# Optimization experiments

Measured on AMD Instinct MI355X. Metric: run time of the kernel, lower is better.

## Reference

```python
import jax, jax.numpy as jnp
import numpy as np

HIDDEN = 512
HEADS = 8
DK = HIDDEN // HEADS  # 64
NEG = -1000000000.0


def setup_inputs() -> dict:
    key = jax.random.key(0)
    ks = jax.random.split(key, 16)
    B, S = 4, 1024
    inp = {
        "q": jax.random.normal(ks[0], (B, S, HIDDEN), jnp.float32),
        "k": jax.random.normal(ks[1], (B, S, HIDDEN), jnp.float32),
        "v": jax.random.normal(ks[2], (B, S, HIDDEN), jnp.float32),
        "attn_bias": jax.random.normal(ks[3], (B, HEADS, S, S), jnp.float32),
        "graph_mask": jax.random.randint(ks[4], (B, 1, S, S), 0, 2, jnp.int32),
        "subsq_mask": jax.random.normal(ks[5], (B, 1, S, S), jnp.float32),
        # linear params (PyTorch Linear: y = x @ W.T + b)
        "Wq": jax.random.normal(ks[6], (HIDDEN, HIDDEN), jnp.float32) * 0.02,
        "bq": jnp.zeros((HIDDEN,), jnp.float32),
        "Wk": jax.random.normal(ks[7], (HIDDEN, HIDDEN), jnp.float32) * 0.02,
        "bk": jnp.zeros((HIDDEN,), jnp.float32),
        "Wv": jax.random.normal(ks[8], (HIDDEN, HIDDEN), jnp.float32) * 0.02,
        "bv": jnp.zeros((HIDDEN,), jnp.float32),
        "Wo": jax.random.normal(ks[9], (HIDDEN, HIDDEN), jnp.float32) * 0.02,
        "bo": jnp.zeros((HIDDEN,), jnp.float32),
    }
    return inp


def reference(q, k, v, attn_bias, graph_mask, subsq_mask, Wq, bq, Wk, bk, Wv, bv, Wo, bo):
    B, S, _ = q.shape
    scale = DK ** (-0.5)
    # projections -> [B, heads, S, d]
    qh = (q @ Wq.T + bq).reshape(B, S, HEADS, DK).transpose(0, 2, 1, 3)
    kh = (k @ Wk.T + bk).reshape(B, S, HEADS, DK).transpose(0, 2, 1, 3)
    vh = (v @ Wv.T + bv).reshape(B, S, HEADS, DK).transpose(0, 2, 1, 3)
    # scaled scores [B, heads, S, S]
    scores = jnp.einsum('bhqd,bhkd->bhqk', qh * scale, kh)
    zero = graph_mask == 0  # [B,1,S,S], broadcasts over heads
    bias = jnp.where(zero, NEG, attn_bias)
    x = scores + bias + subsq_mask
    x = jnp.where(zero, NEG, x)
    attn = jax.nn.softmax(x, axis=-1)
    out = jnp.einsum('bhqk,bhkd->bhqd', attn, vh)
    out = out.transpose(0, 2, 1, 3).reshape(B, S, HEADS * DK)
    return out @ Wo.T + bo
```

## Files before the change

### kernel.cpp

```cpp
#include <hip/hip_runtime.h>

#define HIDDEN 512
#define HEADS 8
#define DK 64
#define S_ 1024
#define NEGV -1000000000.0f

typedef _Float16 half8 __attribute__((ext_vector_type(8)));
typedef _Float16 half4 __attribute__((ext_vector_type(4)));
typedef _Float16 half2_t __attribute__((ext_vector_type(2)));
typedef float f32x4 __attribute__((ext_vector_type(4)));
typedef float f32x2 __attribute__((ext_vector_type(2)));
typedef int i32x4 __attribute__((ext_vector_type(4)));

__device__ __forceinline__ void gload16(const void* g, void* l) {
  __builtin_amdgcn_global_load_lds(
      (const __attribute__((address_space(1))) unsigned int*)g,
      (__attribute__((address_space(3))) unsigned int*)l, 16, 0, 0);
}

__global__ __launch_bounds__(256) void cvt3(const float* __restrict__ a0,
                                            const float* __restrict__ a1,
                                            const float* __restrict__ a2,
                                            _Float16* o0, _Float16* o1, _Float16* o2) {
  const float* src = blockIdx.y == 0 ? a0 : (blockIdx.y == 1 ? a1 : a2);
  _Float16* dst = blockIdx.y == 0 ? o0 : (blockIdx.y == 1 ? o1 : o2);
  int i = (blockIdx.x * 256 + threadIdx.x) * 4;
  float4 v = *(const float4*)(src + i);
  half4 h = {(_Float16)v.x, (_Float16)v.y, (_Float16)v.z, (_Float16)v.w};
  *(half4*)(dst + i) = h;
}

__global__ __launch_bounds__(256) void cvt4(const float* __restrict__ a0,
                                            const float* __restrict__ a1,
                                            const float* __restrict__ a2,
                                            const float* __restrict__ a3,
                                            _Float16* o0, _Float16* o1, _Float16* o2, _Float16* o3) {
  const float* src = blockIdx.y == 0 ? a0 : (blockIdx.y == 1 ? a1 : (blockIdx.y == 2 ? a2 : a3));
  _Float16* dst = blockIdx.y == 0 ? o0 : (blockIdx.y == 1 ? o1 : (blockIdx.y == 2 ? o2 : o3));
  int i = (blockIdx.x * 256 + threadIdx.x) * 4;
  float4 v = *(const float4*)(src + i);
  half4 h = {(_Float16)v.x, (_Float16)v.y, (_Float16)v.z, (_Float16)v.w};
  *(half4*)(dst + i) = h;
}

__global__ __launch_bounds__(256) void fusemask(const int* __restrict__ gm,
                                                const float* __restrict__ sq,
                                                _Float16* __restrict__ msk) {
  int i = (blockIdx.x * 256 + threadIdx.x) * 4;
  i32x4 g = *(const i32x4*)(gm + i);
  f32x4 s = *(const f32x4*)(sq + i);
  half4 o;
#pragma unroll
  for (int j = 0; j < 4; j++)
    o[j] = (_Float16)(g[j] == 0 ? -30000.0f : s[j]);
  *(half4*)(msk + i) = o;
}

__global__ __launch_bounds__(256) void proj_qkv2(
    const _Float16* __restrict__ q16, const _Float16* __restrict__ k16,
    const _Float16* __restrict__ v16,
    const _Float16* __restrict__ wq, const _Float16* __restrict__ wk,
    const _Float16* __restrict__ wv,
    const float* __restrict__ bq, const float* __restrict__ bk,
    const float* __restrict__ bv,
    _Float16* __restrict__ qh, _Float16* __restrict__ kh, _Float16* __restrict__ vt) {
  int m0 = blockIdx.x * 64;
  int nb = blockIdx.y;
  int which = nb >> 3;
  int n0 = (nb & 7) * 64;
  const _Float16* X = which == 0 ? q16 : (which == 1 ? k16 : v16);
  const _Float16* W = which == 0 ? wq : (which == 1 ? wk : wv);
  const float* bias = which == 0 ? bq : (which == 1 ? bk : bv);

  int tid = threadIdx.x;
  int wave = tid >> 6, lane = tid & 63;
  int r16 = lane & 15, quad = lane >> 4;

  __shared__ __align__(16) char SM[25600];
  _Float16(*T)[72] = (_Float16(*)[72])(SM + 16384);

  int rl = lane >> 2;
  int ku = lane & 3;
  int kup = ku ^ ((rl >> 1) & 3);

  const _Float16* Xg = X + (size_t)(m0 + wave * 16 + rl) * HIDDEN + kup * 8;
  const _Float16* Wg = W + (size_t)(n0 + wave * 16 + rl) * HIDDEN + kup * 8;

  auto stage = [&](int k0, int buf) __attribute__((always_inline)) {
    gload16(Xg + k0, SM + buf * 4096 + wave * 1024);
    gload16(Wg + k0, SM + 8192 + buf * 4096 + wave * 1024);
  };

  f32x4 acc[4] = {};
  stage(0, 0);
  int sw = (r16 >> 1) & 3;

  for (int t = 0; t < 16; t++) {
    int k0n = (t < 15) ? (t + 1) * 32 : 0;
    stage(k0n, (t + 1) & 1);
    asm volatile("s_waitcnt vmcnt(2)" ::: "memory");
    __builtin_amdgcn_sched_barrier(0);
    __builtin_amdgcn_s_barrier();

    int buf = t & 1;
    const _Float16* XT = (const _Float16*)(SM + buf * 4096);
    const _Float16* WT = (const _Float16*)(SM + 8192 + buf * 4096);
    half8 a = *(const half8*)&XT[(wave * 16 + r16) * 32 + ((quad ^ sw) << 3)];
#pragma unroll
    for (int nt = 0; nt < 4; nt++) {
      half8 bfr = *(const half8*)&WT[(nt * 16 + r16) * 32 + ((quad ^ sw) << 3)];
      acc[nt] = __builtin_amdgcn_mfma_f32_16x16x32_f16(a, bfr, acc[nt], 0, 0, 0);
    }
    __builtin_amdgcn_s_barrier();
  }
  asm volatile("s_waitcnt vmcnt(0)" ::: "memory");

  if (which < 2) {
    _Float16* OUT = which == 0 ? qh : kh;
    float scale = which == 0 ? 0.125f : 1.0f;
#pragma unroll
    for (int nt = 0; nt < 4; nt++) {
      int gcol = n0 + nt * 16 + r16;
      float bv_ = bias[gcol];
      int h = gcol >> 6, d = gcol & 63;
#pragma unroll
      for (int r = 0; r < 4; r++) {
        int grow = m0 + wave * 16 + quad * 4 + r;
        int bb = grow >> 10, s = grow & 1023;
        float val = (acc[nt][r] + bv_) * scale;
        OUT[((bb * HEADS + h) * S_ + s) * DK + d] = (_Float16)val;
      }
    }
  } else {
#pragma unroll
    for (int nt = 0; nt < 4; nt++) {
      int lc = nt * 16 + r16;
      float bv_ = bias[n0 + lc];
#pragma unroll
      for (int r = 0; r < 4; r++) {
        int lr = wave * 16 + quad * 4 + r;
        T[lr][lc] = (_Float16)(acc[nt][r] + bv_);
      }
    }
    __syncthreads();
    int dl = tid >> 2;
    int s4 = (tid & 3) * 16;
    _Float16 tmp[16];
#pragma unroll
    for (int i = 0; i < 16; i++) tmp[i] = T[s4 + i][dl];
    int h = n0 >> 6;
    int bb = m0 >> 10;
    int s0 = m0 & 1023;
    _Float16* p = vt + ((bb * HEADS + h) * DK + dl) * S_ + s0 + s4;
    *(half8*)(p) = *(half8*)(tmp);
    *(half8*)(p + 8) = *(half8*)(tmp + 8);
  }
}

__global__ __launch_bounds__(256) void attn8(
    const _Float16* __restrict__ qh, const _Float16* __restrict__ kh,
    const _Float16* __restrict__ vt,
    const float* __restrict__ attn_bias, const _Float16* __restrict__ msk,
    _Float16* __restrict__ ao) {
  int id = blockIdx.x;
  int bh = (((id >> 3) & 3) << 3) | (id & 7);
  int qtile = id >> 5;
  int b = bh >> 3, h = bh & 7;
  int tid = threadIdx.x;
  int wave = tid >> 6, lane = tid & 63;
  int col = lane & 15, quad = lane >> 4;
  int q0w = qtile * 64 + wave * 16;
  int q = q0w + col;
  int xr = col & 7;
  int lr8 = lane >> 3;
  int u8 = (lane & 7) ^ lr8;

  __shared__ __align__(16) char SMEM[46080];
  _Float16* Klds = (_Float16*)SMEM;
  _Float16* Vlds = (_Float16*)(SMEM + 8192);
  char* bws = SMEM + 16384 + wave * 4096;
  char* mws = SMEM + 32768 + wave * 2048;
  float* Bw = (float*)bws;
  _Float16* Mw = (_Float16*)mws;
  unsigned(*P2)[16][20] = (unsigned(*)[16][20])(SMEM + 40960);

  const _Float16* Q = qh + ((size_t)bh * S_ + q) * DK;
  const _Float16* K = kh + (size_t)bh * S_ * DK;
  const _Float16* V = vt + (size_t)bh * DK * S_;
  const float* BIrow = attn_bias + ((size_t)bh * S_ + q0w) * S_;
  const _Float16* MSrow = msk + ((size_t)b * S_ + q0w) * S_;

  half8 qf0 = *(const half8*)(Q + quad * 8);
  half8 qf1 = *(const half8*)(Q + 32 + quad * 8);

  f32x4 acc[4] = {};
  float m_r = -1e38f, l_r = 0.0f;

  for (int t = 0; t < 16; t++) {
    int kb = t * 64;
#pragma unroll
    for (int cc = 0; cc < 2; cc++) {
      int c = wave + cc * 4;
      int row = c * 8 + lr8;
      gload16(K + (size_t)(kb + row) * DK + u8 * 8, SMEM + c * 1024);
    }
#pragma unroll
    for (int cc = 0; cc < 2; cc++) {
      int c = wave + cc * 4;
      int row = c * 8 + lr8;
      gload16(V + (size_t)row * S_ + kb + u8 * 8, SMEM + 8192 + c * 1024);
    }
#pragma unroll
    for (int c = 0; c < 4; c++) {
      int row = c * 4 + (lane >> 4);
      int ju = (lane & 15) ^ (row & 7);
      gload16(BIrow + (size_t)row * S_ + kb + ju * 4, bws + c * 1024);
    }
#pragma unroll
    for (int c = 0; c < 2; c++) {
      int row = c * 8 + lr8;
      gload16(MSrow + (size_t)row * S_ + kb + u8 * 8, mws + c * 1024);
    }
    asm volatile("s_waitcnt vmcnt(0)" ::: "memory");
    __builtin_amdgcn_sched_barrier(0);
    __builtin_amdgcn_s_barrier();

#pragma unroll
    for (int hf = 0; hf < 2; hf++) {
      int kcl = hf * 32;
      int R0 = kcl + col, R1 = kcl + 16 + col;
      half8 kf00 = *(const half8*)&Klds[R0 * 64 + ((quad ^ xr) << 3)];
      half8 kf01 = *(const half8*)&Klds[R0 * 64 + (((quad + 4) ^ xr) << 3)];
      half8 kf10 = *(const half8*)&Klds[R1 * 64 + ((quad ^ xr) << 3)];
      half8 kf11 = *(const half8*)&Klds[R1 * 64 + (((quad + 4) ^ xr) << 3)];

      int ku = (kcl >> 3) + quad;
      half8 vf0 = *(const half8*)&Vlds[(0 * 16 + col) * 64 + ((ku ^ xr) << 3)];
      half8 vf1 = *(const half8*)&Vlds[(1 * 16 + col) * 64 + ((ku ^ xr) << 3)];
      half8 vf2 = *(const half8*)&Vlds[(2 * 16 + col) * 64 + ((ku ^ xr) << 3)];
      half8 vf3 = *(const half8*)&Vlds[(3 * 16 + col) * 64 + ((ku ^ xr) << 3)];

      int jb = kcl >> 2;
      f32x4 bi0 = *(const f32x4*)&Bw[col * 64 + (((jb + quad) ^ xr) << 2)];
      f32x4 bi1 = *(const f32x4*)&Bw[col * 64 + (((jb + 4 + quad) ^ xr) << 2)];
      int jm = (kcl >> 3) + (quad >> 1);
      half4 mk0 = *(const half4*)&Mw[col * 64 + ((jm ^ xr) << 3) + (quad & 1) * 4];
      half4 mk1 = *(const half4*)&Mw[col * 64 + (((jm + 2) ^ xr) << 3) + (quad & 1) * 4];

      f32x4 s0 = {}, s1 = {};
      s0 = __builtin_amdgcn_mfma_f32_16x16x32_f16(kf00, qf0, s0, 0, 0, 0);
      s0 = __builtin_amdgcn_mfma_f32_16x16x32_f16(kf01, qf1, s0, 0, 0, 0);
      s1 = __builtin_amdgcn_mfma_f32_16x16x32_f16(kf10, qf0, s1, 0, 0, 0);
      s1 = __builtin_amdgcn_mfma_f32_16x16x32_f16(kf11, qf1, s1, 0, 0, 0);

      float x0[4], x1[4];
#pragma unroll
      for (int r = 0; r < 4; r++) {
        x0[r] = s0[r] + bi0[r] + (float)mk0[r];
        x1[r] = s1[r] + bi1[r] + (float)mk1[r];
      }

      float mx = fmaxf(fmaxf(fmaxf(x0[0], x0[1]), fmaxf(x0[2], x0[3])),
                       fmaxf(fmaxf(x1[0], x1[1]), fmaxf(x1[2], x1[3])));
      mx = fmaxf(mx, __shfl_xor(mx, 16));
      mx = fmaxf(mx, __shfl_xor(mx, 32));
      float mnew = fmaxf(m_r, mx);
      float f = __expf(m_r - mnew);
      float p0[4], p1[4];
      float ps = 0.0f;
#pragma unroll
      for (int r = 0; r < 4; r++) {
        p0[r] = __expf(x0[r] - mnew);
        p1[r] = __expf(x1[r] - mnew);
        ps += p0[r] + p1[r];
      }
      ps += __shfl_xor(ps, 16);
      ps += __shfl_xor(ps, 32);
      l_r = l_r * f + ps;
      m_r = mnew;
#pragma unroll
      for (int nt = 0; nt < 4; nt++) acc[nt] *= f;

      half2_t c0 = {(_Float16)p0[0], (_Float16)p0[1]};
      half2_t c1 = {(_Float16)p0[2], (_Float16)p0[3]};
      half2_t c2 = {(_Float16)p1[0], (_Float16)p1[1]};
      half2_t c3 = {(_Float16)p1[2], (_Float16)p1[3]};
      P2[wave][col][quad * 2 + 0] = __builtin_bit_cast(unsigned, c0);
      P2[wave][col][quad * 2 + 1] = __builtin_bit_cast(unsigned, c1);
      P2[wave][col][8 + quad * 2 + 0] = __builtin_bit_cast(unsigned, c2);
      P2[wave][col][8 + quad * 2 + 1] = __builtin_bit_cast(unsigned, c3);

      half8 pf = *(const half8*)&P2[wave][col][quad * 4];

      acc[0] = __builtin_amdgcn_mfma_f32_16x16x32_f16(vf0, pf, acc[0], 0, 0, 0);
      acc[1] = __builtin_amdgcn_mfma_f32_16x16x32_f16(vf1, pf, acc[1], 0, 0, 0);
      acc[2] = __builtin_amdgcn_mfma_f32_16x16x32_f16(vf2, pf, acc[2], 0, 0, 0);
      acc[3] = __builtin_amdgcn_mfma_f32_16x16x32_f16(vf3, pf, acc[3], 0, 0, 0);
    }
    __builtin_amdgcn_s_barrier();
  }

  float linv = 1.0f / l_r;
  _Float16* aop = ao + (size_t)(b * S_ + q) * HIDDEN + h * DK;
#pragma unroll
  for (int nt = 0; nt < 4; nt++)
#pragma unroll
    for (int rp = 0; rp < 2; rp++) {
      int d = nt * 16 + quad * 4 + rp * 2;
      half2_t o = {(_Float16)(acc[nt][rp * 2] * linv),
                   (_Float16)(acc[nt][rp * 2 + 1] * linv)};
      *(half2_t*)(aop + d) = o;
    }
}

__global__ __launch_bounds__(256) void out_proj2(
    const _Float16* __restrict__ ao, const _Float16* __restrict__ wo,
    const float* __restrict__ bo, float* __restrict__ out) {
  int m0 = blockIdx.x * 64;
  int n0 = blockIdx.y * 64;
  int tid = threadIdx.x, wave = tid >> 6, lane = tid & 63;
  int r16 = lane & 15, quad = lane >> 4;

  __shared__ __align__(16) char SM[16384];
  int rl = lane >> 2;
  int ku = lane & 3;
  int kup = ku ^ ((rl >> 1) & 3);

  const _Float16* Xg = ao + (size_t)(m0 + wave * 16 + rl) * HIDDEN + kup * 8;
  const _Float16* Wg = wo + (size_t)(n0 + wave * 16 + rl) * HIDDEN + kup * 8;

  auto stage = [&](int k0, int buf) __attribute__((always_inline)) {
    gload16(Xg + k0, SM + buf * 4096 + wave * 1024);
    gload16(Wg + k0, SM + 8192 + buf * 4096 + wave * 1024);
  };

  f32x4 acc[4] = {};
  stage(0, 0);
  int sw = (r16 >> 1) & 3;

  for (int t = 0; t < 16; t++) {
    int k0n = (t < 15) ? (t + 1) * 32 : 0;
    stage(k0n, (t + 1) & 1);
    asm volatile("s_waitcnt vmcnt(2)" ::: "memory");
    __builtin_amdgcn_sched_barrier(0);
    __builtin_amdgcn_s_barrier();

    int buf = t & 1;
    const _Float16* XT = (const _Float16*)(SM + buf * 4096);
    const _Float16* WT = (const _Float16*)(SM + 8192 + buf * 4096);
    half8 a = *(const half8*)&XT[(wave * 16 + r16) * 32 + ((quad ^ sw) << 3)];
#pragma unroll
    for (int nt = 0; nt < 4; nt++) {
      half8 bfr = *(const half8*)&WT[(nt * 16 + r16) * 32 + ((quad ^ sw) << 3)];
      acc[nt] = __builtin_amdgcn_mfma_f32_16x16x32_f16(a, bfr, acc[nt], 0, 0, 0);
    }
    __builtin_amdgcn_s_barrier();
  }
  asm volatile("s_waitcnt vmcnt(0)" ::: "memory");

#pragma unroll
  for (int nt = 0; nt < 4; nt++) {
    int gcol = n0 + nt * 16 + r16;
    float bv_ = bo[gcol];
#pragma unroll
    for (int r = 0; r < 4; r++) {
      int grow = m0 + wave * 16 + quad * 4 + r;
      out[grow * HIDDEN + gcol] = acc[nt][r] + bv_;
    }
  }
}

extern "C" void kernel_launch(void* const* d_in, const int* in_sizes, int n_in,
                              void* d_out, int out_size, void* d_ws, size_t ws_size,
                              hipStream_t stream) {
  const float* q = (const float*)d_in[0];
  const float* k = (const float*)d_in[1];
  const float* v = (const float*)d_in[2];
  const float* attn_bias = (const float*)d_in[3];
  const int* gmask = (const int*)d_in[4];
  const float* subsq = (const float*)d_in[5];
  const float* Wq = (const float*)d_in[6];
  const float* bq = (const float*)d_in[7];
  const float* Wk = (const float*)d_in[8];
  const float* bk = (const float*)d_in[9];
  const float* Wv = (const float*)d_in[10];
  const float* bv = (const float*)d_in[11];
  const float* Wo = (const float*)d_in[12];
  const float* bo = (const float*)d_in[13];

  char* ws = (char*)d_ws;
  _Float16* q16 = (_Float16*)(ws + 0);
  _Float16* k16 = (_Float16*)(ws + 4194304);
  _Float16* v16 = (_Float16*)(ws + 8388608);
  _Float16* wq16 = (_Float16*)(ws + 12582912);
  _Float16* wk16 = (_Float16*)(ws + 13107200);
  _Float16* wv16 = (_Float16*)(ws + 13631488);
  _Float16* wo16 = (_Float16*)(ws + 14155776);
  _Float16* qhb = (_Float16*)(ws + 14680064);
  _Float16* khb = (_Float16*)(ws + 18874368);
  _Float16* vtb = (_Float16*)(ws + 23068672);
  _Float16* aob = (_Float16*)(ws + 27262976);
  _Float16* msk16 = (_Float16*)(ws + 0);

  cvt3<<<dim3(2048, 3), 256, 0, stream>>>(q, k, v, q16, k16, v16);
  cvt4<<<dim3(256, 4), 256, 0, stream>>>(Wq, Wk, Wv, Wo, wq16, wk16, wv16, wo16);
  proj_qkv2<<<dim3(64, 24), 256, 0, stream>>>(q16, k16, v16, wq16, wk16, wv16,
                                              bq, bk, bv, qhb, khb, vtb);
  fusemask<<<dim3(4096), 256, 0, stream>>>(gmask, subsq, msk16);
  attn8<<<dim3(512), 256, 0, stream>>>(qhb, khb, vtb, attn_bias, msk16, aob);
  out_proj2<<<dim3(64, 8), 256, 0, stream>>>(aob, wo16, bo, (float*)d_out);
}
```

Baseline: 85.65 us.

## Double-buffer attention K/V/bias/mask tiles with 512-thread blocks covering 128 queries

The attention kernel now uses 8 waves per block, each block handling 128 query rows, so every K/V tile is shared by twice as many queries. All staged tiles (K, V, bias, mask) are double-buffered in LDS. The loads for the next key tile are issued before the current tile is computed, and a partial vmcnt wait keeps them in flight. This aims to hide global-load latency and halve K/V traffic per query, at the cost of about 138KB of LDS (one block per CU) and half as many blocks. The final iteration also prefetches a redundant wrap-around tile.

```diff
diff --git a/kernel.cpp b/kernel.cpp
--- a/kernel.cpp
+++ b/kernel.cpp
@@ -158,7 +158,7 @@
   }
 }
 
-__global__ __launch_bounds__(256) void attn8(
+__global__ __launch_bounds__(512) void attn13(
     const _Float16* __restrict__ qh, const _Float16* __restrict__ kh,
     const _Float16* __restrict__ vt,
     const float* __restrict__ attn_bias, const _Float16* __restrict__ msk,
@@ -170,20 +170,14 @@
   int tid = threadIdx.x;
   int wave = tid >> 6, lane = tid & 63;
   int col = lane & 15, quad = lane >> 4;
-  int q0w = qtile * 64 + wave * 16;
+  int q0w = qtile * 128 + wave * 16;
   int q = q0w + col;
   int xr = col & 7;
   int lr8 = lane >> 3;
   int u8 = (lane & 7) ^ lr8;
 
-  __shared__ __align__(16) char SMEM[46080];
-  _Float16* Klds = (_Float16*)SMEM;
-  _Float16* Vlds = (_Float16*)(SMEM + 8192);
-  char* bws = SMEM + 16384 + wave * 4096;
-  char* mws = SMEM + 32768 + wave * 2048;
-  float* Bw = (float*)bws;
-  _Float16* Mw = (_Float16*)mws;
-  unsigned(*P2)[16][20] = (unsigned(*)[16][20])(SMEM + 40960);
+  __shared__ __align__(16) char SMEM[141312];
+  unsigned(*P2)[16][20] = (unsigned(*)[16][20])(SMEM + 131072);
 
   const _Float16* Q = qh + ((size_t)bh * S_ + q) * DK;
   const _Float16* K = kh + (size_t)bh * S_ * DK;
@@ -197,34 +191,44 @@
   f32x4 acc[4] = {};
   float m_r = -1e38f, l_r = 0.0f;
 
-  for (int t = 0; t < 16; t++) {
-    int kb = t * 64;
-#pragma unroll
-    for (int cc = 0; cc < 2; cc++) {
-      int c = wave + cc * 4;
-      int row = c * 8 + lr8;
-      gload16(K + (size_t)(kb + row) * DK + u8 * 8, SMEM + c * 1024);
-    }
-#pragma unroll
-    for (int cc = 0; cc < 2; cc++) {
-      int c = wave + cc * 4;
-      int row = c * 8 + lr8;
-      gload16(V + (size_t)row * S_ + kb + u8 * 8, SMEM + 8192 + c * 1024);
+  auto stage_clump = [&](int tt, int buf) __attribute__((always_inline)) {
+    int kb = tt * 64;
+    {
+      int row = wave * 8 + lr8;
+      gload16(K + (size_t)(kb + row) * DK + u8 * 8,
+              SMEM + buf * 8192 + wave * 1024);
+      gload16(V + (size_t)row * S_ + kb + u8 * 8,
+              SMEM + 16384 + buf * 8192 + wave * 1024);
     }
 #pragma unroll
     for (int c = 0; c < 4; c++) {
       int row = c * 4 + (lane >> 4);
       int ju = (lane & 15) ^ (row & 7);
-      gload16(BIrow + (size_t)row * S_ + kb + ju * 4, bws + c * 1024);
+      gload16(BIrow + (size_t)row * S_ + kb + ju * 4,
+              SMEM + 32768 + buf * 32768 + wave * 4096 + c * 1024);
     }
 #pragma unroll
     for (int c = 0; c < 2; c++) {
       int row = c * 8 + lr8;
-      gload16(MSrow + (size_t)row * S_ + kb + u8 * 8, mws + c * 1024);
-    }
-    asm volatile("s_waitcnt vmcnt(0)" ::: "memory");
+      gload16(MSrow + (size_t)row * S_ + kb + u8 * 8,
+              SMEM + 98304 + buf * 16384 + wave * 2048 + c * 1024);
+    }
+  };
+
+  stage_clump(0, 0);
+
+  for (int t = 0; t < 16; t++) {
+    stage_clump((t + 1) & 15, (t + 1) & 1);
+
+    asm volatile("s_waitcnt vmcnt(8)" ::: "memory");
     __builtin_amdgcn_sched_barrier(0);
     __builtin_amdgcn_s_barrier();
+
+    int buf = t & 1;
+    _Float16* Klds = (_Float16*)(SMEM + buf * 8192);
+    _Float16* Vlds = (_Float16*)(SMEM + 16384 + buf * 8192);
+    float* Bw = (float*)(SMEM + 32768 + buf * 32768 + wave * 4096);
+    _Float16* Mw = (_Float16*)(SMEM + 98304 + buf * 16384 + wave * 2048);
 
 #pragma unroll
     for (int hf = 0; hf < 2; hf++) {
@@ -300,6 +304,7 @@
     }
     __builtin_amdgcn_s_barrier();
   }
+  asm volatile("s_waitcnt vmcnt(0)" ::: "memory");
 
   float linv = 1.0f / l_r;
   _Float16* aop = ao + (size_t)(b * S_ + q) * HIDDEN + h * DK;
@@ -408,6 +413,6 @@
   proj_qkv2<<<dim3(64, 24), 256, 0, stream>>>(q16, k16, v16, wq16, wk16, wv16,
                                               bq, bk, bv, qhb, khb, vtb);
   fusemask<<<dim3(4096), 256, 0, stream>>>(gmask, subsq, msk16);
-  attn8<<<dim3(512), 256, 0, stream>>>(qhb, khb, vtb, attn_bias, msk16, aob);
+  attn13<<<dim3(256), 512, 0, stream>>>(qhb, khb, vtb, attn_bias, msk16, aob);
   out_proj2<<<dim3(64, 8), 256, 0, stream>>>(aob, wo16, bo, (float*)d_out);
 }
```

New measurement: 82.33 us. 1.04x faster.
